# Kernel tuning notes

Measured on AMD Instinct MI355X. Metric: run time of the kernel, lower is better.

The kernel has to match this reference:

```python
import jax, jax.numpy as jnp
import numpy as np

B, N, D, H = 2, 2048, 1024, 16
HD = D // H
SCALE = HD ** -0.5

def setup_inputs() -> dict:
    key = jax.random.key(0)
    ks = jax.random.split(key, 5)
    x = jax.random.normal(ks[0], (B, N, D), dtype=jnp.float32)
    w_qkv = jax.random.normal(ks[1], (D, 3 * D), dtype=jnp.float32) * (1.0 / np.sqrt(D))
    b_qkv = jnp.zeros((3 * D,), dtype=jnp.float32)
    w_proj = jax.random.normal(ks[2], (D, D), dtype=jnp.float32) * (1.0 / np.sqrt(D))
    b_proj = jnp.zeros((D,), dtype=jnp.float32)
    return {"x": x, "w_qkv": w_qkv, "b_qkv": b_qkv, "w_proj": w_proj, "b_proj": b_proj}

def reference(x, w_qkv, b_qkv, w_proj, b_proj):
    # qkv projection: [B,N,3D] -> [3,B,H,N,HD]
    qkv = (x @ w_qkv + b_qkv).reshape(B, N, 3, H, HD).transpose(2, 0, 3, 1, 4)
    q, k, v = qkv[0], qkv[1], qkv[2]
    attn = jnp.einsum('bhnd,bhmd->bhnm', q, k) * SCALE  # [B,H,N,N]
    attn = jax.nn.softmax(attn, axis=-1)
    out = jnp.einsum('bhnm,bhmd->bhnd', attn, v)  # [B,H,N,HD]
    out = out.transpose(0, 2, 1, 3).reshape(B, N, D)
    return out @ w_proj + b_proj
```

## Files before the change

### kernel.cpp

```cpp
#include <hip/hip_runtime.h>
#include <cmath>

constexpr int Bb  = 2;
constexpr int Nn  = 2048;
constexpr int Dd  = 1024;
constexpr int Hh  = 16;
constexpr int HDd = 64;

#define QSCALE 0.18033688011112042f

typedef __attribute__((ext_vector_type(8))) _Float16 f16x8;
typedef __attribute__((ext_vector_type(2))) __fp16   fp16x2;
typedef __attribute__((ext_vector_type(4))) float    f32x4;

__device__ inline unsigned short f2h(float f) {
  _Float16 h = (_Float16)f;
  union { _Float16 h; unsigned short u; } v; v.h = h; return v.u;
}
__device__ inline unsigned cvt_pk_f16(float x, float y) {
  union { fp16x2 h; unsigned u; } v;
  v.h = __builtin_amdgcn_cvt_pkrtz(x, y);
  return v.u;
}
__device__ inline float fexp2(float x) {
  float r;
  asm("v_exp_f32 %0, %1" : "=v"(r) : "v"(x));
  return r;
}
__device__ inline void gload16(const void* g, void* l) {
  __builtin_amdgcn_global_load_lds((const __attribute__((address_space(1))) void*)g,
                                   (__attribute__((address_space(3))) void*)l, 16, 0, 0);
}

__global__ __launch_bounds__(256) void prep(
    const float* __restrict__ X, const float* __restrict__ Wq,
    const float* __restrict__ Wp,
    unsigned short* __restrict__ Xf, unsigned short* __restrict__ Bqt,
    unsigned short* __restrict__ Bpt)
{
  const int bid = blockIdx.x;
  const int t = threadIdx.x;

  if (bid < 2048) {
    const size_t i = ((size_t)bid * 256 + t) * 8;
    float4 u0 = *(const float4*)(X + i);
    float4 u1 = *(const float4*)(X + i + 4);
    ushort4 a, b;
    a.x = f2h(u0.x); a.y = f2h(u0.y); a.z = f2h(u0.z); a.w = f2h(u0.w);
    b.x = f2h(u1.x); b.y = f2h(u1.y); b.z = f2h(u1.z); b.w = f2h(u1.w);
    *(ushort4*)(Xf + i)     = a;
    *(ushort4*)(Xf + i + 4) = b;
    return;
  }

  __shared__ float T[64][65];
  const float* W; unsigned short* Wt; int Nd, n0, k0;
  if (bid < 2816) {
    const int b2 = bid - 2048;
    W = Wq; Wt = Bqt; Nd = 3 * Dd;
    n0 = (b2 % 48) * 64; k0 = (b2 / 48) * 64;
  } else {
    const int b3 = bid - 2816;
    W = Wp; Wt = Bpt; Nd = Dd;
    n0 = (b3 & 15) * 64; k0 = (b3 >> 4) * 64;
  }
  const int Kd = Dd;
#pragma unroll
  for (int i = 0; i < 4; ++i) {
    int idx = t + 256 * i;
    int r = idx >> 4, c4 = (idx & 15) * 4;
    float4 v = *(const float4*)(W + (size_t)(k0 + r) * Nd + n0 + c4);
    T[c4 + 0][r] = v.x; T[c4 + 1][r] = v.y;
    T[c4 + 2][r] = v.z; T[c4 + 3][r] = v.w;
  }
  __syncthreads();
#pragma unroll
  for (int i = 0; i < 4; ++i) {
    int idx = t + 256 * i;
    int nr = idx >> 4, kc = (idx & 15) * 4;
    ushort4 hv;
    hv.x = f2h(T[nr][kc + 0]); hv.y = f2h(T[nr][kc + 1]);
    hv.z = f2h(T[nr][kc + 2]); hv.w = f2h(T[nr][kc + 3]);
    *(ushort4*)(Wt + (size_t)(n0 + nr) * Kd + k0 + kc) = hv;
  }
}

template<int EPI, int BM>
__global__ __launch_bounds__(256, 4) void gemm_f16(
    const unsigned short* __restrict__ Ag,
    const unsigned short* __restrict__ Bg,
    const float* __restrict__ bias,
    float* __restrict__ Cout,
    unsigned short* __restrict__ Qf, unsigned short* __restrict__ Kf,
    unsigned short* __restrict__ Vtf,
    int Nsz, int Ksz, int gridM)
{
  __shared__ __align__(16) unsigned short A_s[BM * 64];
  __shared__ __align__(16) unsigned short B_s[8192];

  constexpr int NB = 4;
  constexpr int NBW = (BM == 128) ? 4 : 2;
  (void)NB;

  const int t    = threadIdx.x;
  const int lane = t & 63, w = t >> 6;
  const int g = lane >> 4, lid = lane & 15;
  const int wr = (BM == 128) ? (w >> 1) : 0;
  const int wcol0 = (BM == 128) ? ((w & 1) * 64) : (w * 32);

  const int nwg = gridDim.x;
  const int per = nwg >> 3;
  const int bid = (blockIdx.x & 7) * per + (blockIdx.x >> 3);
  const int by = bid % gridM, bx = bid / gridM;
  const int row0 = by * BM, col0 = bx * 128;

  f32x4 acc[4][NBW];
#pragma unroll
  for (int i = 0; i < 4; ++i)
#pragma unroll
    for (int j = 0; j < NBW; ++j) acc[i][j] = f32x4{0.f, 0.f, 0.f, 0.f};

  const int sg8 = ((lane & 7) ^ (lane >> 3)) * 8;
  const int rl8 = lane >> 3;

  for (int k0 = 0; k0 < Ksz; k0 += 64) {
    if (BM == 128) {
#pragma unroll
      for (int q = 0; q < 4; ++q) {
        const int oct = w * 4 + q;
        const int r = oct * 8 + rl8;
        gload16(Ag + (size_t)(row0 + r) * Ksz + k0 + sg8, A_s + oct * 512);
        gload16(Bg + (size_t)(col0 + r) * Ksz + k0 + sg8, B_s + oct * 512);
      }
    } else {
#pragma unroll
      for (int q = 0; q < 2; ++q) {
        const int oct = w * 2 + q;
        const int r = oct * 8 + rl8;
        gload16(Ag + (size_t)(row0 + r) * Ksz + k0 + sg8, A_s + oct * 512);
      }
#pragma unroll
      for (int q = 0; q < 4; ++q) {
        const int oct = w * 4 + q;
        const int r = oct * 8 + rl8;
        gload16(Bg + (size_t)(col0 + r) * Ksz + k0 + sg8, B_s + oct * 512);
      }
    }
    __syncthreads();

#pragma unroll
    for (int kk = 0; kk < 2; ++kk) {
      f16x8 a[4], b[NBW];
#pragma unroll
      for (int mb = 0; mb < 4; ++mb) {
        const int r = wr * 64 + mb * 16 + lid;
        const int off = r * 64 + (((kk * 4 + g) ^ (r & 7)) << 3);
        a[mb] = *(const f16x8*)(A_s + off);
      }
#pragma unroll
      for (int nb = 0; nb < NBW; ++nb) {
        const int c = wcol0 + nb * 16 + lid;
        const int off = c * 64 + (((kk * 4 + g) ^ (c & 7)) << 3);
        b[nb] = *(const f16x8*)(B_s + off);
      }
#pragma unroll
      for (int mb = 0; mb < 4; ++mb)
#pragma unroll
        for (int nb = 0; nb < NBW; ++nb)
          acc[mb][nb] = __builtin_amdgcn_mfma_f32_16x16x32_f16(a[mb], b[nb], acc[mb][nb], 0, 0, 0);
    }
    __syncthreads();
  }

#pragma unroll
  for (int nb = 0; nb < NBW; ++nb) {
    const int cg = col0 + wcol0 + nb * 16 + lid;
    const float bv = bias[cg];
    if (EPI == 0) {
#pragma unroll
      for (int mb = 0; mb < 4; ++mb)
#pragma unroll
        for (int reg = 0; reg < 4; ++reg) {
          int nrow = row0 + wr * 64 + mb * 16 + 4 * g + reg;
          Cout[(size_t)nrow * Nsz + cg] = acc[mb][nb][reg] + bv;
        }
    } else {
      const int region = cg >> 10;
      const int h  = (cg & 1023) >> 6;
      const int hd = cg & 63;
      const int b2 = row0 >> 11;
      const int bh_ = b2 * Hh + h;
      const float sc = (region == 0) ? QSCALE : 1.0f;
#pragma unroll
      for (int mb = 0; mb < 4; ++mb) {
        const int nt0 = (row0 & 2047) + wr * 64 + mb * 16 + 4 * g;
        float cc[4];
#pragma unroll
        for (int reg = 0; reg < 4; ++reg) cc[reg] = (acc[mb][nb][reg] + bv) * sc;
        if (region == 2) {
          const int ns = (nt0 & ~31) | ((nt0 & 12) << 1) | ((nt0 & 16) >> 2);
          ushort4 vv;
          vv.x = f2h(cc[0]); vv.y = f2h(cc[1]);
          vv.z = f2h(cc[2]); vv.w = f2h(cc[3]);
          *(ushort4*)(Vtf + ((size_t)bh_ * HDd + hd) * Nn + ns) = vv;
        } else {
          unsigned short* P = (region == 0) ? Qf : Kf;
#pragma unroll
          for (int reg = 0; reg < 4; ++reg)
            P[((size_t)bh_ * Nn + nt0 + reg) * HDd + hd] = f2h(cc[reg]);
        }
      }
    }
  }
}

__global__ __launch_bounds__(256, 2) void attn_mfma(
    const unsigned short* __restrict__ Qf, const unsigned short* __restrict__ Kf,
    const unsigned short* __restrict__ Vt,
    unsigned short* __restrict__ Of)
{
  __shared__ __align__(16) unsigned short Kf_s[16384];
  __shared__ __align__(16) unsigned short Vt_s[16384];

  const int t    = threadIdx.x;
  const int lane = t & 63, w = t >> 6;
  const int g    = lane >> 4, lid = lane & 15;

  const int hw = blockIdx.x;
  const int bh = (hw & 7) * 4 + ((hw >> 3) & 3);
  const int q0 = (hw >> 5) * 128;
  const int b_ = bh >> 4, h_ = bh & 15;

  const size_t kvbase = (size_t)bh * Nn * HDd;

  const int qrowA = q0 + w * 16 + lid;
  const unsigned short* qpA = Qf + kvbase + (size_t)qrowA * HDd + g * 8;
  f16x8 qa0 = *(const f16x8*)(qpA);
  f16x8 qa1 = *(const f16x8*)(qpA + 32);
  const unsigned short* qpB = qpA + (size_t)64 * HDd;
  f16x8 qb0 = *(const f16x8*)(qpB);
  f16x8 qb1 = *(const f16x8*)(qpB + 32);

  f16x8 vones;
#pragma unroll
  for (int i = 0; i < 8; ++i) vones[i] = (_Float16)1.0f;

  f32x4 oA[4], oB[4];
  f32x4 olA = f32x4{0.f, 0.f, 0.f, 0.f};
  f32x4 olB = f32x4{0.f, 0.f, 0.f, 0.f};
#pragma unroll
  for (int i = 0; i < 4; ++i) { oA[i] = f32x4{0.f,0.f,0.f,0.f}; oB[i] = f32x4{0.f,0.f,0.f,0.f}; }

  const int sg8 = ((lane & 7) ^ (lane >> 3)) * 8;

  auto stage = [&](int buf, int kv0) {
#pragma unroll
    for (int q = 0; q < 8; ++q) {
      const int idx = w * 8 + q;
      if (idx < 16) {
        const int r = idx * 8 + (lane >> 3);
        gload16(Kf + kvbase + (size_t)(kv0 + r) * HDd + sg8,
                Kf_s + buf * 8192 + idx * 512);
      } else {
        const int qd = idx - 16;
        const int r = qd * 4 + (lane >> 4);
        const int srcc = (lane & 15) ^ (r & 15);
        gload16(Vt + kvbase + (size_t)r * Nn + kv0 + srcc * 8,
                Vt_s + buf * 8192 + qd * 512);
      }
    }
  };

  stage(0, 0);
  int cur = 0;
  const int NT = Nn / 128;

  union PU { unsigned u[4]; f16x8 v; };

  for (int tt = 0; tt < NT; ++tt) {
    __syncthreads();
    if (tt + 1 < NT) stage(cur ^ 1, (tt + 1) * 128);

    const int kb = cur * 8192;

    f32x4 sA[8], sB[8];
#pragma unroll
    for (int jbb = 0; jbb < 8; ++jbb) { sA[jbb] = f32x4{0.f,0.f,0.f,0.f}; sB[jbb] = f32x4{0.f,0.f,0.f,0.f}; }
    __builtin_amdgcn_s_setprio(1);
#pragma unroll
    for (int jbb = 0; jbb < 8; ++jbb) {
      const int row = jbb * 16 + lid;
      const int rs = kb + row * 64;
      const int sw = row & 7;
      f16x8 kf0 = *(const f16x8*)&Kf_s[rs + ((g       ^ sw)) * 8];
      f16x8 kf1 = *(const f16x8*)&Kf_s[rs + (((4 + g) ^ sw)) * 8];
      sA[jbb] = __builtin_amdgcn_mfma_f32_16x16x32_f16(kf0, qa0, sA[jbb], 0, 0, 0);
      sA[jbb] = __builtin_amdgcn_mfma_f32_16x16x32_f16(kf1, qa1, sA[jbb], 0, 0, 0);
      sB[jbb] = __builtin_amdgcn_mfma_f32_16x16x32_f16(kf0, qb0, sB[jbb], 0, 0, 0);
      sB[jbb] = __builtin_amdgcn_mfma_f32_16x16x32_f16(kf1, qb1, sB[jbb], 0, 0, 0);
    }
    __builtin_amdgcn_s_setprio(0);

#pragma unroll
    for (int h = 0; h < 2; ++h) {
#pragma unroll
      for (int jb = 0; jb < 4; ++jb)
#pragma unroll
        for (int reg = 0; reg < 4; ++reg) {
          sA[h * 4 + jb][reg] = fexp2(sA[h * 4 + jb][reg]);
          sB[h * 4 + jb][reg] = fexp2(sB[h * 4 + jb][reg]);
        }

      PU pA0, pA1, pB0, pB1;
#pragma unroll
      for (int jb = 0; jb < 2; ++jb) {
        pA0.u[2 * jb + 0] = cvt_pk_f16(sA[h * 4 + jb][0], sA[h * 4 + jb][1]);
        pA0.u[2 * jb + 1] = cvt_pk_f16(sA[h * 4 + jb][2], sA[h * 4 + jb][3]);
        pA1.u[2 * jb + 0] = cvt_pk_f16(sA[h * 4 + 2 + jb][0], sA[h * 4 + 2 + jb][1]);
        pA1.u[2 * jb + 1] = cvt_pk_f16(sA[h * 4 + 2 + jb][2], sA[h * 4 + 2 + jb][3]);
        pB0.u[2 * jb + 0] = cvt_pk_f16(sB[h * 4 + jb][0], sB[h * 4 + jb][1]);
        pB0.u[2 * jb + 1] = cvt_pk_f16(sB[h * 4 + jb][2], sB[h * 4 + jb][3]);
        pB1.u[2 * jb + 0] = cvt_pk_f16(sB[h * 4 + 2 + jb][0], sB[h * 4 + 2 + jb][1]);
        pB1.u[2 * jb + 1] = cvt_pk_f16(sB[h * 4 + 2 + jb][2], sB[h * 4 + 2 + jb][3]);
      }

      __builtin_amdgcn_s_setprio(1);
      olA = __builtin_amdgcn_mfma_f32_16x16x32_f16(pA0.v, vones, olA, 0, 0, 0);
      olA = __builtin_amdgcn_mfma_f32_16x16x32_f16(pA1.v, vones, olA, 0, 0, 0);
      olB = __builtin_amdgcn_mfma_f32_16x16x32_f16(pB0.v, vones, olB, 0, 0, 0);
      olB = __builtin_amdgcn_mfma_f32_16x16x32_f16(pB1.v, vones, olB, 0, 0, 0);
#pragma unroll
      for (int cb = 0; cb < 4; ++cb) {
        const int vrow = cb * 16 + lid;
        const int vs = kb + vrow * 128;
        const int sw = vrow & 15;
        f16x8 vb0 = *(const f16x8*)&Vt_s[vs + (((8 * h + g)     ^ sw)) * 8];
        f16x8 vb1 = *(const f16x8*)&Vt_s[vs + (((8 * h + 4 + g) ^ sw)) * 8];
        oA[cb] = __builtin_amdgcn_mfma_f32_16x16x32_f16(pA0.v, vb0, oA[cb], 0, 0, 0);
        oA[cb] = __builtin_amdgcn_mfma_f32_16x16x32_f16(pA1.v, vb1, oA[cb], 0, 0, 0);
        oB[cb] = __builtin_amdgcn_mfma_f32_16x16x32_f16(pB0.v, vb0, oB[cb], 0, 0, 0);
        oB[cb] = __builtin_amdgcn_mfma_f32_16x16x32_f16(pB1.v, vb1, oB[cb], 0, 0, 0);
      }
      __builtin_amdgcn_s_setprio(0);
    }
    cur ^= 1;
  }

  const size_t obaseA = ((size_t)(b_ * Nn + q0 + w * 16)) * Dd + h_ * 64;
  const size_t obaseB = obaseA + (size_t)64 * Dd;
#pragma unroll
  for (int reg = 0; reg < 4; ++reg) {
    const int row = 4 * g + reg;
    const float ivA = 1.0f / olA[reg];
    const float ivB = 1.0f / olB[reg];
#pragma unroll
    for (int cb = 0; cb < 4; ++cb) {
      Of[obaseA + (size_t)row * Dd + cb * 16 + lid] = f2h(oA[cb][reg] * ivA);
      Of[obaseB + (size_t)row * Dd + cb * 16 + lid] = f2h(oB[cb][reg] * ivB);
    }
  }
}

extern "C" void kernel_launch(void* const* d_in, const int* in_sizes, int n_in,
                              void* d_out, int out_size, void* d_ws, size_t ws_size,
                              hipStream_t stream)
{
  const float* x      = (const float*)d_in[0];
  const float* w_qkv  = (const float*)d_in[1];
  const float* b_qkv  = (const float*)d_in[2];
  const float* w_proj = (const float*)d_in[3];
  const float* b_proj = (const float*)d_in[4];
  float* outp = (float*)d_out;

  unsigned char* ws = (unsigned char*)d_ws;
  const size_t MB = 1ull << 20;
  unsigned short* Xf  = (unsigned short*)(ws +  0 * MB);
  unsigned short* Bqt = (unsigned short*)(ws +  8 * MB);
  unsigned short* Qf  = (unsigned short*)(ws + 14 * MB);
  unsigned short* Kf  = (unsigned short*)(ws + 22 * MB);
  unsigned short* Vtf = (unsigned short*)(ws + 30 * MB);
  unsigned short* Ofb = (unsigned short*)(ws + 38 * MB);
  unsigned short* Bpt = (unsigned short*)(ws + 46 * MB);

  const int M = Bb * Nn;

  prep<<<dim3(3072), 256, 0, stream>>>(x, w_qkv, w_proj, Xf, Bqt, Bpt);

  gemm_f16<1, 128><<<dim3((3 * Dd / 128) * (M / 128)), 256, 0, stream>>>(
      Xf, Bqt, b_qkv, nullptr, Qf, Kf, Vtf, 3 * Dd, Dd, M / 128);

  attn_mfma<<<dim3((Nn / 128) * Bb * Hh), 256, 0, stream>>>(Qf, Kf, Vtf, Ofb);

  gemm_f16<0, 64><<<dim3((Dd / 128) * (M / 64)), 256, 0, stream>>>(
      Ofb, Bpt, b_proj, outp, nullptr, nullptr, nullptr, Dd, Dd, M / 64);
}
```

Baseline: 100.2 us.

## Interleave exp2 softmax work with QK and PV MFMAs in attention loop

```diff
diff --git a/kernel.cpp b/kernel.cpp
--- a/kernel.cpp
+++ b/kernel.cpp
@@ -98,9 +98,7 @@
   __shared__ __align__(16) unsigned short A_s[BM * 64];
   __shared__ __align__(16) unsigned short B_s[8192];
 
-  constexpr int NB = 4;
   constexpr int NBW = (BM == 128) ? 4 : 2;
-  (void)NB;
 
   const int t    = threadIdx.x;
   const int lane = t & 63, w = t >> 6;
@@ -286,9 +284,10 @@
     f32x4 sA[8], sB[8];
 #pragma unroll
     for (int jbb = 0; jbb < 8; ++jbb) { sA[jbb] = f32x4{0.f,0.f,0.f,0.f}; sB[jbb] = f32x4{0.f,0.f,0.f,0.f}; }
+
     __builtin_amdgcn_s_setprio(1);
 #pragma unroll
-    for (int jbb = 0; jbb < 8; ++jbb) {
+    for (int jbb = 0; jbb < 4; ++jbb) {
       const int row = jbb * 16 + lid;
       const int rs = kb + row * 64;
       const int sw = row & 7;
@@ -301,48 +300,91 @@
     }
     __builtin_amdgcn_s_setprio(0);
 
-#pragma unroll
-    for (int h = 0; h < 2; ++h) {
-#pragma unroll
-      for (int jb = 0; jb < 4; ++jb)
-#pragma unroll
-        for (int reg = 0; reg < 4; ++reg) {
-          sA[h * 4 + jb][reg] = fexp2(sA[h * 4 + jb][reg]);
-          sB[h * 4 + jb][reg] = fexp2(sB[h * 4 + jb][reg]);
-        }
-
-      PU pA0, pA1, pB0, pB1;
-#pragma unroll
-      for (int jb = 0; jb < 2; ++jb) {
-        pA0.u[2 * jb + 0] = cvt_pk_f16(sA[h * 4 + jb][0], sA[h * 4 + jb][1]);
-        pA0.u[2 * jb + 1] = cvt_pk_f16(sA[h * 4 + jb][2], sA[h * 4 + jb][3]);
-        pA1.u[2 * jb + 0] = cvt_pk_f16(sA[h * 4 + 2 + jb][0], sA[h * 4 + 2 + jb][1]);
-        pA1.u[2 * jb + 1] = cvt_pk_f16(sA[h * 4 + 2 + jb][2], sA[h * 4 + 2 + jb][3]);
-        pB0.u[2 * jb + 0] = cvt_pk_f16(sB[h * 4 + jb][0], sB[h * 4 + jb][1]);
-        pB0.u[2 * jb + 1] = cvt_pk_f16(sB[h * 4 + jb][2], sB[h * 4 + jb][3]);
-        pB1.u[2 * jb + 0] = cvt_pk_f16(sB[h * 4 + 2 + jb][0], sB[h * 4 + 2 + jb][1]);
-        pB1.u[2 * jb + 1] = cvt_pk_f16(sB[h * 4 + 2 + jb][2], sB[h * 4 + 2 + jb][3]);
-      }
-
-      __builtin_amdgcn_s_setprio(1);
-      olA = __builtin_amdgcn_mfma_f32_16x16x32_f16(pA0.v, vones, olA, 0, 0, 0);
-      olA = __builtin_amdgcn_mfma_f32_16x16x32_f16(pA1.v, vones, olA, 0, 0, 0);
-      olB = __builtin_amdgcn_mfma_f32_16x16x32_f16(pB0.v, vones, olB, 0, 0, 0);
-      olB = __builtin_amdgcn_mfma_f32_16x16x32_f16(pB1.v, vones, olB, 0, 0, 0);
-#pragma unroll
-      for (int cb = 0; cb < 4; ++cb) {
-        const int vrow = cb * 16 + lid;
-        const int vs = kb + vrow * 128;
-        const int sw = vrow & 15;
-        f16x8 vb0 = *(const f16x8*)&Vt_s[vs + (((8 * h + g)     ^ sw)) * 8];
-        f16x8 vb1 = *(const f16x8*)&Vt_s[vs + (((8 * h + 4 + g) ^ sw)) * 8];
-        oA[cb] = __builtin_amdgcn_mfma_f32_16x16x32_f16(pA0.v, vb0, oA[cb], 0, 0, 0);
-        oA[cb] = __builtin_amdgcn_mfma_f32_16x16x32_f16(pA1.v, vb1, oA[cb], 0, 0, 0);
-        oB[cb] = __builtin_amdgcn_mfma_f32_16x16x32_f16(pB0.v, vb0, oB[cb], 0, 0, 0);
-        oB[cb] = __builtin_amdgcn_mfma_f32_16x16x32_f16(pB1.v, vb1, oB[cb], 0, 0, 0);
-      }
-      __builtin_amdgcn_s_setprio(0);
-    }
+    PU pA0, pA1, pB0, pB1;
+#pragma unroll
+    for (int j = 0; j < 4; ++j) {
+      const int jbb = 4 + j;
+      const int row = jbb * 16 + lid;
+      const int rs = kb + row * 64;
+      const int sw = row & 7;
+      f16x8 kf0 = *(const f16x8*)&Kf_s[rs + ((g       ^ sw)) * 8];
+      f16x8 kf1 = *(const f16x8*)&Kf_s[rs + (((4 + g) ^ sw)) * 8];
+      sA[jbb] = __builtin_amdgcn_mfma_f32_16x16x32_f16(kf0, qa0, sA[jbb], 0, 0, 0);
+      sA[jbb] = __builtin_amdgcn_mfma_f32_16x16x32_f16(kf1, qa1, sA[jbb], 0, 0, 0);
+      sB[jbb] = __builtin_amdgcn_mfma_f32_16x16x32_f16(kf0, qb0, sB[jbb], 0, 0, 0);
+      sB[jbb] = __builtin_amdgcn_mfma_f32_16x16x32_f16(kf1, qb1, sB[jbb], 0, 0, 0);
+#pragma unroll
+      for (int reg = 0; reg < 4; ++reg) {
+        sA[j][reg] = fexp2(sA[j][reg]);
+        sB[j][reg] = fexp2(sB[j][reg]);
+      }
+      if (j == 1) {
+        pA0.u[0] = cvt_pk_f16(sA[0][0], sA[0][1]); pA0.u[1] = cvt_pk_f16(sA[0][2], sA[0][3]);
+        pA0.u[2] = cvt_pk_f16(sA[1][0], sA[1][1]); pA0.u[3] = cvt_pk_f16(sA[1][2], sA[1][3]);
+        pB0.u[0] = cvt_pk_f16(sB[0][0], sB[0][1]); pB0.u[1] = cvt_pk_f16(sB[0][2], sB[0][3]);
+        pB0.u[2] = cvt_pk_f16(sB[1][0], sB[1][1]); pB0.u[3] = cvt_pk_f16(sB[1][2], sB[1][3]);
+      }
+      if (j == 3) {
+        pA1.u[0] = cvt_pk_f16(sA[2][0], sA[2][1]); pA1.u[1] = cvt_pk_f16(sA[2][2], sA[2][3]);
+        pA1.u[2] = cvt_pk_f16(sA[3][0], sA[3][1]); pA1.u[3] = cvt_pk_f16(sA[3][2], sA[3][3]);
+        pB1.u[0] = cvt_pk_f16(sB[2][0], sB[2][1]); pB1.u[1] = cvt_pk_f16(sB[2][2], sB[2][3]);
+        pB1.u[2] = cvt_pk_f16(sB[3][0], sB[3][1]); pB1.u[3] = cvt_pk_f16(sB[3][2], sB[3][3]);
+      }
+    }
+
+    PU qA0, qA1, qB0, qB1;
+    olA = __builtin_amdgcn_mfma_f32_16x16x32_f16(pA0.v, vones, olA, 0, 0, 0);
+    olA = __builtin_amdgcn_mfma_f32_16x16x32_f16(pA1.v, vones, olA, 0, 0, 0);
+    olB = __builtin_amdgcn_mfma_f32_16x16x32_f16(pB0.v, vones, olB, 0, 0, 0);
+    olB = __builtin_amdgcn_mfma_f32_16x16x32_f16(pB1.v, vones, olB, 0, 0, 0);
+#pragma unroll
+    for (int cb = 0; cb < 4; ++cb) {
+      const int vrow = cb * 16 + lid;
+      const int vs = kb + vrow * 128;
+      const int sw = vrow & 15;
+      f16x8 vb0 = *(const f16x8*)&Vt_s[vs + ((g       ^ sw)) * 8];
+      f16x8 vb1 = *(const f16x8*)&Vt_s[vs + (((4 + g) ^ sw)) * 8];
+      oA[cb] = __builtin_amdgcn_mfma_f32_16x16x32_f16(pA0.v, vb0, oA[cb], 0, 0, 0);
+      oA[cb] = __builtin_amdgcn_mfma_f32_16x16x32_f16(pA1.v, vb1, oA[cb], 0, 0, 0);
+      oB[cb] = __builtin_amdgcn_mfma_f32_16x16x32_f16(pB0.v, vb0, oB[cb], 0, 0, 0);
+      oB[cb] = __builtin_amdgcn_mfma_f32_16x16x32_f16(pB1.v, vb1, oB[cb], 0, 0, 0);
+#pragma unroll
+      for (int reg = 0; reg < 4; ++reg) {
+        sA[4 + cb][reg] = fexp2(sA[4 + cb][reg]);
+        sB[4 + cb][reg] = fexp2(sB[4 + cb][reg]);
+      }
+      if (cb == 1) {
+        qA0.u[0] = cvt_pk_f16(sA[4][0], sA[4][1]); qA0.u[1] = cvt_pk_f16(sA[4][2], sA[4][3]);
+        qA0.u[2] = cvt_pk_f16(sA[5][0], sA[5][1]); qA0.u[3] = cvt_pk_f16(sA[5][2], sA[5][3]);
+        qB0.u[0] = cvt_pk_f16(sB[4][0], sB[4][1]); qB0.u[1] = cvt_pk_f16(sB[4][2], sB[4][3]);
+        qB0.u[2] = cvt_pk_f16(sB[5][0], sB[5][1]); qB0.u[3] = cvt_pk_f16(sB[5][2], sB[5][3]);
+      }
+      if (cb == 3) {
+        qA1.u[0] = cvt_pk_f16(sA[6][0], sA[6][1]); qA1.u[1] = cvt_pk_f16(sA[6][2], sA[6][3]);
+        qA1.u[2] = cvt_pk_f16(sA[7][0], sA[7][1]); qA1.u[3] = cvt_pk_f16(sA[7][2], sA[7][3]);
+        qB1.u[0] = cvt_pk_f16(sB[6][0], sB[6][1]); qB1.u[1] = cvt_pk_f16(sB[6][2], sB[6][3]);
+        qB1.u[2] = cvt_pk_f16(sB[7][0], sB[7][1]); qB1.u[3] = cvt_pk_f16(sB[7][2], sB[7][3]);
+      }
+    }
+
+    __builtin_amdgcn_s_setprio(1);
+    olA = __builtin_amdgcn_mfma_f32_16x16x32_f16(qA0.v, vones, olA, 0, 0, 0);
+    olA = __builtin_amdgcn_mfma_f32_16x16x32_f16(qA1.v, vones, olA, 0, 0, 0);
+    olB = __builtin_amdgcn_mfma_f32_16x16x32_f16(qB0.v, vones, olB, 0, 0, 0);
+    olB = __builtin_amdgcn_mfma_f32_16x16x32_f16(qB1.v, vones, olB, 0, 0, 0);
+#pragma unroll
+    for (int cb = 0; cb < 4; ++cb) {
+      const int vrow = cb * 16 + lid;
+      const int vs = kb + vrow * 128;
+      const int sw = vrow & 15;
+      f16x8 vb0 = *(const f16x8*)&Vt_s[vs + (((8 + g)  ^ sw)) * 8];
+      f16x8 vb1 = *(const f16x8*)&Vt_s[vs + (((12 + g) ^ sw)) * 8];
+      oA[cb] = __builtin_amdgcn_mfma_f32_16x16x32_f16(qA0.v, vb0, oA[cb], 0, 0, 0);
+      oA[cb] = __builtin_amdgcn_mfma_f32_16x16x32_f16(qA1.v, vb1, oA[cb], 0, 0, 0);
+      oB[cb] = __builtin_amdgcn_mfma_f32_16x16x32_f16(qB0.v, vb0, oB[cb], 0, 0, 0);
+      oB[cb] = __builtin_amdgcn_mfma_f32_16x16x32_f16(qB1.v, vb1, oB[cb], 0, 0, 0);
+    }
+    __builtin_amdgcn_s_setprio(0);
     cur ^= 1;
   }
 
```

New measurement: 100.6 us. About the same (+0.4%).
